# Optimization experiments

Hardware: AMD Instinct MI355X
Metric: run time of the kernel (lower is better)

## Reference

```python
import jax, jax.numpy as jnp
import numpy as np

P_ITER = 30   # Krylov iterations (p_iter=30 in source)
N_PROBE = 100 # stochastic probe vectors (t=100 in source)


def setup_inputs() -> dict:
    N, t, r = 8192, N_PROBE, 256
    key = jax.random.key(0)
    kA, ky, kz = jax.random.split(key, 3)
    # Well-conditioned SPD kernel + noise matrix: K = A A^T / r + I
    A = jax.random.normal(kA, (N, r), dtype=jnp.float32)
    Knn_noise = (A @ A.T) / r + jnp.eye(N, dtype=jnp.float32)
    y = jax.random.normal(ky, (N, 1), dtype=jnp.float32)
    # Rademacher probes (||z||^2 = N exactly)
    Z = jnp.where(jax.random.normal(kz, (N, t)) >= 0, 1.0, -1.0).astype(jnp.float32)
    return {"Knn_noise": Knn_noise, "y": y, "Z": Z}


def _batched_cg(K, B, p_iter):
    """Batched conjugate gradients on K X = B, tracking Lanczos coefficients.
    B: [N, M]. Returns X [N, M], alphas [p, M], betas [p, M]."""
    X = jnp.zeros_like(B)
    R = B
    P = B
    rs = jnp.sum(R * R, axis=0)  # [M]

    def step(carry, _):
        X, R, P, rs = carry
        V = K @ P                               # [N, M] dense matvec (GEMM)
        pv = jnp.sum(P * V, axis=0)             # [M]
        alpha = rs / pv
        X = X + alpha * P
        R = R - alpha * V
        rs_new = jnp.sum(R * R, axis=0)
        beta = rs_new / rs
        P = R + beta * P
        return (X, R, P, rs_new), (alpha, beta)

    (X, _, _, _), (alphas, betas) = jax.lax.scan(step, (X, R, P, rs), None, length=p_iter)
    return X, alphas, betas


def _slq_logdet(alphas, betas, N):
    """Stochastic Lanczos quadrature logdet from CG coefficients.
    alphas, betas: [p, t] (one column per probe)."""
    inv_a = 1.0 / alphas                                   # [p, t]
    diag = inv_a.at[1:].add(betas[:-1] / alphas[:-1])      # T diagonal  [p, t]
    off = jnp.sqrt(betas[:-1]) / alphas[:-1]               # T off-diag  [p-1, t]

    def make_T(d, o):
        return jnp.diag(d) + jnp.diag(o, 1) + jnp.diag(o, -1)

    Ts = jax.vmap(make_T, in_axes=(1, 1))(diag, off)       # [t, p, p]
    lam, V = jnp.linalg.eigh(Ts)                           # small p x p eig per probe
    lam = jnp.maximum(lam, 1e-12)
    # z^T log(K) z ~= ||z||^2 * e1^T Vexp log(Lam) V^T e1 ; ||z||^2 = N (Rademacher)
    quad = jnp.sum(V[:, 0, :] ** 2 * jnp.log(lam), axis=1)  # [t]
    return N * jnp.mean(quad)


def reference(Knn_noise, y, Z):
    N = y.shape[0]
    B = jnp.concatenate([y, Z], axis=1)                    # solve + probes together
    X, alphas, betas = _batched_cg(Knn_noise, B, P_ITER)
    Knn_i_y = X[:, :1]                                     # K^{-1} y
    log_det = _slq_logdet(alphas[:, 1:], betas[:, 1:], N)  # SLQ logdet from probes
    two_pi = jnp.asarray(2.0 * np.pi, dtype=y.dtype)
    return -0.5 * (y.T @ Knn_i_y) - 0.5 * log_det - N * 0.5 * jnp.log(two_pi)
```

## Files before the change

### kernel.cpp

```cpp
#include <hip/hip_runtime.h>
#include <hip/hip_fp16.h>

#define NN 8192
#define NCOLS 101
#define CPW 112
#define BN 128
#define BM 128
#define KSPL 8
#define KCH (NN / KSPL)
#define NSTEP (KCH / 128)
#define PITER 30
#define PVLD 104
#define NSMALL 23424

typedef __attribute__((ext_vector_type(4))) float f32x4;

__device__ __forceinline__ void async_copy16(const void* g, void* l) {
  __builtin_amdgcn_global_load_lds(
      (const __attribute__((address_space(1))) unsigned int*)g,
      (__attribute__((address_space(3))) unsigned int*)l, 16, 0, 0);
}

__device__ __forceinline__ unsigned int pack_fp8x4(float x, float y, float z, float w) {
  unsigned int v = __builtin_amdgcn_cvt_pk_fp8_f32(x, y, 0, false);
  v = __builtin_amdgcn_cvt_pk_fp8_f32(z, w, v, true);
  return v;
}

__device__ __forceinline__ float block_sum(float v) {
  __shared__ float sw[4];
  __syncthreads();
  #pragma unroll
  for (int o = 32; o > 0; o >>= 1) v += __shfl_down(v, o);
  int w = threadIdx.x >> 6;
  if ((threadIdx.x & 63) == 0) sw[w] = v;
  __syncthreads();
  float r = 0.f;
  if (threadIdx.x < 4) r = sw[threadIdx.x];
  r += __shfl_down(r, 2);
  r += __shfl_down(r, 1);
  return r;
}

__global__ __launch_bounds__(256, 2) void gemm_kernel(
    const unsigned char* __restrict__ Kbt,
    const unsigned char* __restrict__ Pb,
    const float* __restrict__ Pf,
    const float* __restrict__ SCit,
    __half* __restrict__ Vp,
    float* __restrict__ pvp) {
  __shared__ __align__(16) unsigned char smem[65536];
  unsigned char* sA = smem;
  unsigned char* sB = smem + 32768;
  float* sC = (float*)smem;

  int bx = blockIdx.x;
  int kz = bx & 7;
  int rb = bx >> 3;
  int tid = threadIdx.x;
  int lane = tid & 63;
  int w = tid >> 6;
  int r0 = rb * BM;
  int k0 = kz * KCH;
  int lrow = lane >> 3;
  int gseg = (lane & 7) ^ lrow;
  int asrc = lrow * 128 + gseg * 16;
  int mm = lane & 15;
  int quad = lane >> 4;
  int q1 = quad >> 1, q0 = quad & 1;
  int wm = w >> 1, wn = w & 1;

  const unsigned char* Apanel = Kbt + ((size_t)bx << 17);

  int aBase[4], aXor[4], bBase[4], bXor[4];
  #pragma unroll
  for (int i = 0; i < 4; ++i) {
    int arow = wm * 64 + i * 16 + mm;
    aBase[i] = arow * 128 + (q0 << 3);
    aXor[i] = (arow & 7) << 4;
    int bcol = wn * 64 + i * 16 + mm;
    bBase[i] = bcol * 128 + (q0 << 3);
    bXor[i] = (bcol & 7) << 4;
  }

  f32x4 acc[4][4];
  #pragma unroll
  for (int i = 0; i < 4; ++i)
    #pragma unroll
    for (int j = 0; j < 4; ++j) acc[i][j] = (f32x4){0.f, 0.f, 0.f, 0.f};

  auto stage = [&](int s, int buf) {
    int kk = k0 + s * 128;
    #pragma unroll
    for (int q = 0; q < 4; ++q) {
      async_copy16(Apanel + (s << 14) + (w * 32 + q * 8) * 128 + asrc,
                   sA + buf * 16384 + (w * 32 + q * 8) * 128);
      async_copy16(Pb + (size_t)(w * 32 + q * 8 + lrow) * NN + kk + gseg * 16,
                   sB + buf * 16384 + (w * 32 + q * 8) * 128);
    }
  };

  stage(0, 0);
  __syncthreads();

  #pragma unroll 2
  for (int s = 0; s < NSTEP; ++s) {
    int cur = s & 1;
    if (s + 1 < NSTEP) stage(s + 1, cur ^ 1);
    const unsigned char* A = sA + cur * 16384;
    const unsigned char* B = sB + cur * 16384;
    #pragma unroll
    for (int kh = 0; kh < 4; ++kh) {
      int s16 = (kh * 2 + q1) << 4;
      long long aF[4], bF[4];
      #pragma unroll
      for (int i = 0; i < 4; ++i) {
        aF[i] = *(const long long*)(A + aBase[i] + (s16 ^ aXor[i]));
        bF[i] = *(const long long*)(B + bBase[i] + (s16 ^ bXor[i]));
      }
      #pragma unroll
      for (int i = 0; i < 4; ++i)
        #pragma unroll
        for (int j = 0; j < 4; ++j)
          acc[i][j] = __builtin_amdgcn_mfma_f32_16x16x32_fp8_fp8(aF[i], bF[j], acc[i][j], 0, 0, 0);
    }
    __syncthreads();
  }
  #pragma unroll
  for (int i = 0; i < 4; ++i)
    #pragma unroll
    for (int j = 0; j < 4; ++j) {
      int ctile = wn * 64 + j * 16;
      if (ctile >= CPW) continue;
      #pragma unroll
      for (int r = 0; r < 4; ++r)
        sC[(wm * 64 + i * 16 + quad * 4 + r) * 113 + ctile + mm] = acc[i][j][r];
    }
  __syncthreads();
  const size_t SPL = (size_t)CPW * NN;
  __half* Vout = Vp + (size_t)kz * SPL;
  for (int idx = tid; idx < BM * CPW; idx += 256) {
    int col = idx >> 7;
    int row = idx & 127;
    if (col < NCOLS)
      Vout[(size_t)col * NN + r0 + row] = __float2half(sC[row * 113 + col] * SCit[col]);
  }
  int rr = tid & 63;
  int g = tid >> 6;
  for (int j = 0; j < 26; ++j) {
    int c = g + j * 4;
    float prod = 0.f;
    if (c < NCOLS)
      prod = (sC[rr * 113 + c] * Pf[(size_t)c * NN + r0 + rr] +
              sC[(rr + 64) * 113 + c] * Pf[(size_t)c * NN + r0 + 64 + rr]) * SCit[c];
    #pragma unroll
    for (int o = 32; o > 0; o >>= 1) prod += __shfl_down(prod, o);
    if (rr == 0 && c < NCOLS) pvp[(size_t)bx * PVLD + c] = prod;
  }
}

__global__ void update1_kernel(const __half* __restrict__ Vp,
                               const float* __restrict__ Pf,
                               float* __restrict__ R,
                               float* __restrict__ X0,
                               const float* __restrict__ pvp,
                               const float* __restrict__ rs,
                               float* __restrict__ rs_new,
                               float* __restrict__ alphas) {
  const size_t SPL = (size_t)CPW * NN;
  __shared__ float s_alpha;
  int c = blockIdx.y;
  int t = threadIdx.x;
  float pvv = pvp[(size_t)t * PVLD + c] + pvp[(size_t)(t + 256) * PVLD + c];
  float pvtot = block_sum(pvv);
  if (t == 0) s_alpha = rs[c] / pvtot;
  __syncthreads();
  float alpha = s_alpha;

  size_t off = (size_t)c * NN + blockIdx.x * 1024 + t * 4;
  float4 v = {0.f, 0.f, 0.f, 0.f};
  #pragma unroll
  for (int sp = 0; sp < KSPL; ++sp) {
    const __half2* p = (const __half2*)(Vp + sp * SPL + off);
    float2 f01 = __half22float2(p[0]);
    float2 f23 = __half22float2(p[1]);
    v.x += f01.x; v.y += f01.y; v.z += f23.x; v.w += f23.y;
  }
  float4 r = *(float4*)(R + off);
  r.x -= alpha * v.x; r.y -= alpha * v.y; r.z -= alpha * v.z; r.w -= alpha * v.w;
  *(float4*)(R + off) = r;
  if (c == 0) {
    size_t xo = blockIdx.x * 1024 + t * 4;
    float4 x = *(float4*)(X0 + xo);
    float4 p = *(const float4*)(Pf + off);
    x.x += alpha * p.x; x.y += alpha * p.y; x.z += alpha * p.z; x.w += alpha * p.w;
    *(float4*)(X0 + xo) = x;
  }
  float rn = r.x * r.x + r.y * r.y + r.z * r.z + r.w * r.w;
  float tot = block_sum(rn);
  if (t == 0) {
    atomicAdd(rs_new + c, tot);
    if (blockIdx.x == 0) alphas[c] = alpha;
  }
}

__global__ void update2_kernel(const float* __restrict__ R,
                               float* __restrict__ P,
                               unsigned char* __restrict__ Pb,
                               const float* __restrict__ rs,
                               const float* __restrict__ rs_new,
                               const float* __restrict__ PNold,
                               float* __restrict__ PNnew,
                               float* __restrict__ SCnew,
                               float* __restrict__ betas) {
  int c = blockIdx.y;
  float rsn = rs_new[c];
  float beta = rsn / rs[c];
  float pnn = rsn + beta * beta * PNold[c];
  float sc = exp2f(roundf(0.5f * log2f(pnn * (1.f / 8192.f))));
  float inv = 1.f / sc;
  size_t off = (size_t)c * NN + blockIdx.x * 1024 + threadIdx.x * 4;
  float4 r = *(const float4*)(R + off);
  float4 p = *(float4*)(P + off);
  p.x = r.x + beta * p.x; p.y = r.y + beta * p.y;
  p.z = r.z + beta * p.z; p.w = r.w + beta * p.w;
  *(float4*)(P + off) = p;
  *(unsigned int*)(Pb + off) = pack_fp8x4(p.x * inv, p.y * inv, p.z * inv, p.w * inv);
  if (threadIdx.x == 0 && blockIdx.x == 0) {
    betas[c] = beta;
    PNnew[c] = pnn;
    SCnew[c] = sc;
  }
}

__global__ void cast_k_kernel(const float* __restrict__ K, unsigned char* __restrict__ Kbt) {
  for (size_t u = (size_t)blockIdx.x * 256 + threadIdx.x; u < (size_t)NN * NN / 16;
       u += (size_t)gridDim.x * 256) {
    size_t d = u * 16;
    int p = (int)(d >> 17);
    int rem = (int)(d & 131071);
    int s = rem >> 14;
    int row = (rem >> 7) & 127;
    int cb = rem & 127;
    int r = (p >> 3) * 128 + row;
    int c = (p & 7) * KCH + s * 128 + cb;
    const float* src = K + (size_t)r * NN + c;
    float4 f0 = *(const float4*)(src);
    float4 f1 = *(const float4*)(src + 4);
    float4 f2 = *(const float4*)(src + 8);
    float4 f3 = *(const float4*)(src + 12);
    uint4 o;
    o.x = pack_fp8x4(f0.x, f0.y, f0.z, f0.w);
    o.y = pack_fp8x4(f1.x, f1.y, f1.z, f1.w);
    o.z = pack_fp8x4(f2.x, f2.y, f2.z, f2.w);
    o.w = pack_fp8x4(f3.x, f3.y, f3.z, f3.w);
    *(uint4*)(Kbt + d) = o;
  }
}

__global__ void init_vec_kernel(const float* __restrict__ y, const float* __restrict__ Z,
                                float* __restrict__ P, float* __restrict__ R,
                                unsigned char* __restrict__ Pb) {
  int c = blockIdx.y;
  int i = blockIdx.x * 256 + threadIdx.x;
  float val = (c == 0) ? y[i] : Z[(size_t)i * 100 + (c - 1)];
  size_t off = (size_t)c * NN + i;
  P[off] = val;
  R[off] = val;
  Pb[off] = (unsigned char)(__builtin_amdgcn_cvt_pk_fp8_f32(val, 0.f, 0, false) & 0xFF);
}

__global__ void init_misc_kernel(float* __restrict__ X0, float* __restrict__ smalls,
                                 unsigned char* __restrict__ Pbpad) {
  const int total = 8192 + NSMALL + 27 * NN;
  for (int t = blockIdx.x * 256 + threadIdx.x; t < total; t += gridDim.x * 256) {
    if (t < 8192) X0[t] = 0.f;
    else if (t < 8192 + NSMALL) smalls[t - 8192] = 0.f;
    else Pbpad[t - (8192 + NSMALL)] = 0;
  }
}

__global__ void init_rs_kernel(const float* __restrict__ y, float* __restrict__ rs0,
                               float* __restrict__ pn0, float* __restrict__ sc0) {
  int t = threadIdx.x;
  float s = 0.f;
  for (int i = t; i < NN; i += 256) { float v = y[i]; s += v * v; }
  float tot = block_sum(s);
  if (t == 0) { rs0[0] = tot; pn0[0] = tot; }
  if (t >= 1 && t <= 100) { rs0[t] = (float)NN; pn0[t] = (float)NN; }
  if (t < 128) sc0[t] = 1.f;
}

__global__ __launch_bounds__(64, 1) void slq_kernel(
    const float* __restrict__ AL, const float* __restrict__ BE,
    float* __restrict__ QP) {
  __shared__ double sd[PITER], se[PITER];
  int lane = threadIdx.x;
  int c = blockIdx.x + 1;
  if (lane < PITER) {
    double a = (double)AL[lane * 128 + c];
    double dd = 1.0 / a;
    if (lane > 0) {
      double ap = (double)AL[(lane - 1) * 128 + c];
      double bp = (double)BE[(lane - 1) * 128 + c];
      dd += bp / ap;
    }
    sd[lane] = dd;
    double ee = 0.0;
    if (lane < PITER - 1) {
      double b = (double)BE[lane * 128 + c];
      ee = sqrt(b) / a;
    }
    se[lane] = ee;
  }
  __syncthreads();
  double d[PITER], e[PITER];
  #pragma unroll
  for (int i = 0; i < PITER; ++i) { d[i] = sd[i]; e[i] = se[i]; }

  float quadk = 0.f;
  if (lane < PITER) {
    double lo = 1e300, hi = -1e300;
    #pragma unroll
    for (int i = 0; i < PITER; ++i) {
      double r = e[i] + (i > 0 ? e[i - 1] : 0.0);
      lo = fmin(lo, d[i] - r);
      hi = fmax(hi, d[i] + r);
    }
    int k = lane;
    for (int it = 0; it < 48; ++it) {
      double mid = 0.5 * (lo + hi);
      int cnt = 0;
      double q = d[0] - mid;
      cnt += (q < 0.0);
      #pragma unroll
      for (int i = 1; i < PITER; ++i) {
        double aq = fabs(q);
        if (aq < 1e-30) q = (q < 0.0) ? -1e-30 : 1e-30;
        q = d[i] - mid - (e[i - 1] * e[i - 1]) / q;
        cnt += (q < 0.0);
      }
      if (cnt > k) hi = mid; else lo = mid;
    }
    double lam = 0.5 * (lo + hi);
    double e0 = fmax(e[0], 1e-150);
    double vprev = 1.0;
    double vcur = (lam - d[0]) / e0;
    double s = 1.0 + vcur * vcur;
    double scale2 = 1.0;
    #pragma unroll
    for (int i = 1; i < PITER - 1; ++i) {
      double ei = fmax(e[i], 1e-150);
      double vnext = ((lam - d[i]) * vcur - e[i - 1] * vprev) / ei;
      if (fabs(vnext) > 1e150) {
        vnext *= 1e-150; vcur *= 1e-150; s *= 1e-300; scale2 *= 1e-300;
      }
      vprev = vcur; vcur = vnext;
      s += vcur * vcur;
    }
    double w = scale2 / s;
    double lc = lam > 1e-12 ? lam : 1e-12;
    quadk = (float)(w * log(lc));
  }
  #pragma unroll
  for (int o = 32; o > 0; o >>= 1) quadk += __shfl_down(quadk, o);
  if (lane == 0) QP[blockIdx.x] = quadk;
}

__global__ void final2_kernel(const float* __restrict__ y, const float* __restrict__ X0,
                              const float* __restrict__ QP, float* __restrict__ out) {
  int t = threadIdx.x;
  float s = 0.f;
  for (int i = t; i < NN; i += 256) s += y[i] * X0[i];
  float ydot = block_sum(s);
  __syncthreads();
  float q = (t < 100) ? QP[t] : 0.f;
  float qsum = block_sum(q);
  if (t == 0) {
    float logdet = (float)NN * (qsum * 0.01f);
    out[0] = -0.5f * ydot - 0.5f * logdet - (float)NN * 0.5f * 1.8378770664093454f;
  }
}

extern "C" void kernel_launch(void* const* d_in, const int* in_sizes, int n_in,
                              void* d_out, int out_size, void* d_ws, size_t ws_size,
                              hipStream_t stream) {
  const float* K = (const float*)d_in[0];
  const float* y = (const float*)d_in[1];
  const float* Z = (const float*)d_in[2];
  float* out = (float*)d_out;
  char* ws = (char*)d_ws;
  if (ws_size < 89796096ull) return;

  unsigned char* Kbt = (unsigned char*)(ws + 0ull);
  unsigned char* Pb = (unsigned char*)(ws + 67108864ull);
  float* P   = (float*)(ws + 68157440ull);
  float* R   = (float*)(ws + 71467008ull);
  __half* Vp = (__half*)(ws + 74776576ull);
  float* X0  = (float*)(ws + 89456640ull);
  float* PVP = (float*)(ws + 89489408ull);
  float* SM  = (float*)(ws + 89702400ull);
  float* RS = SM;
  float* AL = SM + 7808;
  float* BE = SM + 11648;
  float* PN = SM + 15488;
  float* SC = SM + 19456;
  float* QP = (float*)(ws + 74776576ull);

  cast_k_kernel<<<8192, 256, 0, stream>>>(K, Kbt);
  init_vec_kernel<<<dim3(32, 101), 256, 0, stream>>>(y, Z, P, R, Pb);
  init_misc_kernel<<<240, 256, 0, stream>>>(X0, SM, Pb + (size_t)NCOLS * NN);
  init_rs_kernel<<<1, 256, 0, stream>>>(y, RS, PN, SC);

  for (int it = 0; it < PITER; ++it) {
    gemm_kernel<<<512, 256, 0, stream>>>(Kbt, Pb, P, SC + it * 128, Vp, PVP);
    update1_kernel<<<dim3(8, 101), 256, 0, stream>>>(Vp, P, R, X0, PVP,
        RS + it * 128, RS + (it + 1) * 128, AL + it * 128);
    update2_kernel<<<dim3(8, 101), 256, 0, stream>>>(R, P, Pb, RS + it * 128,
        RS + (it + 1) * 128, PN + it * 128, PN + (it + 1) * 128,
        SC + (it + 1) * 128, BE + it * 128);
  }
  slq_kernel<<<100, 64, 0, stream>>>(AL, BE, QP);
  final2_kernel<<<1, 256, 0, stream>>>(y, X0, QP, out);
}
```

Before: 2.032 ms.

## Fuse CG update kernels into one per-column block and merge init kernels

Replaces the two per-iteration update kernels with a single kernel using one 1024-thread block per column. That block reduces the full residual norm itself, so there is no atomicAdd and no second pass that rereads R. It also skips the P update on the last iteration. The four init kernels are merged into one launch. This removes a kernel launch per iteration and an R round-trip through memory, at the cost of only 101 blocks, which may leave many CUs idle for the bandwidth-bound update.

Result: faster. 1.916 ms (-5.7%).

```diff
diff --git a/kernel.cpp b/kernel.cpp
--- a/kernel.cpp
+++ b/kernel.cpp
@@ -11,7 +11,6 @@
 #define NSTEP (KCH / 128)
 #define PITER 30
 #define PVLD 104
-#define NSMALL 23424
 
 typedef __attribute__((ext_vector_type(4))) float f32x4;
 
@@ -37,6 +36,23 @@
   __syncthreads();
   float r = 0.f;
   if (threadIdx.x < 4) r = sw[threadIdx.x];
+  r += __shfl_down(r, 2);
+  r += __shfl_down(r, 1);
+  return r;
+}
+
+__device__ __forceinline__ float block_sum1024(float v) {
+  __shared__ float sw[16];
+  __syncthreads();
+  #pragma unroll
+  for (int o = 32; o > 0; o >>= 1) v += __shfl_down(v, o);
+  int w = threadIdx.x >> 6;
+  if ((threadIdx.x & 63) == 0) sw[w] = v;
+  __syncthreads();
+  float r = 0.f;
+  if (threadIdx.x < 16) r = sw[threadIdx.x];
+  r += __shfl_down(r, 8);
+  r += __shfl_down(r, 4);
   r += __shfl_down(r, 2);
   r += __shfl_down(r, 1);
   return r;
@@ -159,83 +175,96 @@
   }
 }
 
-__global__ void update1_kernel(const __half* __restrict__ Vp,
-                               const float* __restrict__ Pf,
-                               float* __restrict__ R,
-                               float* __restrict__ X0,
-                               const float* __restrict__ pvp,
-                               const float* __restrict__ rs,
-                               float* __restrict__ rs_new,
-                               float* __restrict__ alphas) {
+__global__ __launch_bounds__(1024, 1) void update_kernel(
+    const __half* __restrict__ Vp, float* __restrict__ P,
+    float* __restrict__ R, float* __restrict__ X0,
+    unsigned char* __restrict__ Pb, const float* __restrict__ pvp,
+    float* __restrict__ SM, int it) {
+  float* RS = SM;
+  float* AL = SM + 7808;
+  float* BE = SM + 11648;
+  float* PN = SM + 15488;
+  float* SC = SM + 19456;
+  __shared__ float sbc[2];
+
+  int c = blockIdx.x;
+  int t = threadIdx.x;
   const size_t SPL = (size_t)CPW * NN;
-  __shared__ float s_alpha;
-  int c = blockIdx.y;
+  size_t base = (size_t)c * NN;
+
+  float pvv = (t < 512) ? pvp[(size_t)t * PVLD + c] : 0.f;
+  float pvtot = block_sum1024(pvv);
+  float rs_old = RS[it * 128 + c];
+  if (t == 0) sbc[0] = rs_old / pvtot;
+  __syncthreads();
+  float alpha = sbc[0];
+
+  float4 rv[2];
+  float rn = 0.f;
+  #pragma unroll
+  for (int j = 0; j < 2; ++j) {
+    size_t off = base + j * 4096 + t * 4;
+    float4 v = {0.f, 0.f, 0.f, 0.f};
+    #pragma unroll
+    for (int sp = 0; sp < KSPL; ++sp) {
+      const __half2* ph = (const __half2*)(Vp + sp * SPL + off);
+      float2 f01 = __half22float2(ph[0]);
+      float2 f23 = __half22float2(ph[1]);
+      v.x += f01.x; v.y += f01.y; v.z += f23.x; v.w += f23.y;
+    }
+    float4 r = *(float4*)(R + off);
+    r.x -= alpha * v.x; r.y -= alpha * v.y;
+    r.z -= alpha * v.z; r.w -= alpha * v.w;
+    *(float4*)(R + off) = r;
+    rv[j] = r;
+    rn += r.x * r.x + r.y * r.y + r.z * r.z + r.w * r.w;
+    if (c == 0) {
+      size_t xo = j * 4096 + t * 4;
+      float4 x = *(float4*)(X0 + xo);
+      float4 p = *(const float4*)(P + off);
+      x.x += alpha * p.x; x.y += alpha * p.y;
+      x.z += alpha * p.z; x.w += alpha * p.w;
+      *(float4*)(X0 + xo) = x;
+    }
+  }
+  float rsn = block_sum1024(rn);
+  if (t == 0) {
+    float beta = rsn / rs_old;
+    float pnn = rsn + beta * beta * PN[it * 128 + c];
+    float sc = exp2f(roundf(0.5f * log2f(pnn * (1.f / 8192.f))));
+    AL[it * 128 + c] = alpha;
+    BE[it * 128 + c] = beta;
+    PN[(it + 1) * 128 + c] = pnn;
+    SC[(it + 1) * 128 + c] = sc;
+    RS[(it + 1) * 128 + c] = rsn;
+    sbc[0] = beta;
+    sbc[1] = 1.f / sc;
+  }
+  __syncthreads();
+  if (it < PITER - 1) {
+    float beta = sbc[0], inv = sbc[1];
+    #pragma unroll
+    for (int j = 0; j < 2; ++j) {
+      size_t off = base + j * 4096 + t * 4;
+      float4 p = *(float4*)(P + off);
+      p.x = rv[j].x + beta * p.x; p.y = rv[j].y + beta * p.y;
+      p.z = rv[j].z + beta * p.z; p.w = rv[j].w + beta * p.w;
+      *(float4*)(P + off) = p;
+      *(unsigned int*)(Pb + off) = pack_fp8x4(p.x * inv, p.y * inv, p.z * inv, p.w * inv);
+    }
+  }
+}
+
+__global__ void init_all(const float* __restrict__ K, const float* __restrict__ y,
+                         const float* __restrict__ Z, unsigned char* __restrict__ Kbt,
+                         unsigned char* __restrict__ Pb, float* __restrict__ P,
+                         float* __restrict__ R, float* __restrict__ X0,
+                         float* __restrict__ SM) {
+  int b = blockIdx.x;
   int t = threadIdx.x;
-  float pvv = pvp[(size_t)t * PVLD + c] + pvp[(size_t)(t + 256) * PVLD + c];
-  float pvtot = block_sum(pvv);
-  if (t == 0) s_alpha = rs[c] / pvtot;
-  __syncthreads();
-  float alpha = s_alpha;
-
-  size_t off = (size_t)c * NN + blockIdx.x * 1024 + t * 4;
-  float4 v = {0.f, 0.f, 0.f, 0.f};
-  #pragma unroll
-  for (int sp = 0; sp < KSPL; ++sp) {
-    const __half2* p = (const __half2*)(Vp + sp * SPL + off);
-    float2 f01 = __half22float2(p[0]);
-    float2 f23 = __half22float2(p[1]);
-    v.x += f01.x; v.y += f01.y; v.z += f23.x; v.w += f23.y;
-  }
-  float4 r = *(float4*)(R + off);
-  r.x -= alpha * v.x; r.y -= alpha * v.y; r.z -= alpha * v.z; r.w -= alpha * v.w;
-  *(float4*)(R + off) = r;
-  if (c == 0) {
-    size_t xo = blockIdx.x * 1024 + t * 4;
-    float4 x = *(float4*)(X0 + xo);
-    float4 p = *(const float4*)(Pf + off);
-    x.x += alpha * p.x; x.y += alpha * p.y; x.z += alpha * p.z; x.w += alpha * p.w;
-    *(float4*)(X0 + xo) = x;
-  }
-  float rn = r.x * r.x + r.y * r.y + r.z * r.z + r.w * r.w;
-  float tot = block_sum(rn);
-  if (t == 0) {
-    atomicAdd(rs_new + c, tot);
-    if (blockIdx.x == 0) alphas[c] = alpha;
-  }
-}
-
-__global__ void update2_kernel(const float* __restrict__ R,
-                               float* __restrict__ P,
-                               unsigned char* __restrict__ Pb,
-                               const float* __restrict__ rs,
-                               const float* __restrict__ rs_new,
-                               const float* __restrict__ PNold,
-                               float* __restrict__ PNnew,
-                               float* __restrict__ SCnew,
-                               float* __restrict__ betas) {
-  int c = blockIdx.y;
-  float rsn = rs_new[c];
-  float beta = rsn / rs[c];
-  float pnn = rsn + beta * beta * PNold[c];
-  float sc = exp2f(roundf(0.5f * log2f(pnn * (1.f / 8192.f))));
-  float inv = 1.f / sc;
-  size_t off = (size_t)c * NN + blockIdx.x * 1024 + threadIdx.x * 4;
-  float4 r = *(const float4*)(R + off);
-  float4 p = *(float4*)(P + off);
-  p.x = r.x + beta * p.x; p.y = r.y + beta * p.y;
-  p.z = r.z + beta * p.z; p.w = r.w + beta * p.w;
-  *(float4*)(P + off) = p;
-  *(unsigned int*)(Pb + off) = pack_fp8x4(p.x * inv, p.y * inv, p.z * inv, p.w * inv);
-  if (threadIdx.x == 0 && blockIdx.x == 0) {
-    betas[c] = beta;
-    PNnew[c] = pnn;
-    SCnew[c] = sc;
-  }
-}
-
-__global__ void cast_k_kernel(const float* __restrict__ K, unsigned char* __restrict__ Kbt) {
-  for (size_t u = (size_t)blockIdx.x * 256 + threadIdx.x; u < (size_t)NN * NN / 16;
-       u += (size_t)gridDim.x * 256) {
+  int gid = b * 256 + t;
+  const int gsz = 512 * 256;
+  for (size_t u = gid; u < (size_t)NN * NN / 16; u += gsz) {
     size_t d = u * 16;
     int p = (int)(d >> 17);
     int rem = (int)(d & 131071);
@@ -256,39 +285,30 @@
     o.w = pack_fp8x4(f3.x, f3.y, f3.z, f3.w);
     *(uint4*)(Kbt + d) = o;
   }
-}
-
-__global__ void init_vec_kernel(const float* __restrict__ y, const float* __restrict__ Z,
-                                float* __restrict__ P, float* __restrict__ R,
-                                unsigned char* __restrict__ Pb) {
-  int c = blockIdx.y;
-  int i = blockIdx.x * 256 + threadIdx.x;
-  float val = (c == 0) ? y[i] : Z[(size_t)i * 100 + (c - 1)];
-  size_t off = (size_t)c * NN + i;
-  P[off] = val;
-  R[off] = val;
-  Pb[off] = (unsigned char)(__builtin_amdgcn_cvt_pk_fp8_f32(val, 0.f, 0, false) & 0xFF);
-}
-
-__global__ void init_misc_kernel(float* __restrict__ X0, float* __restrict__ smalls,
-                                 unsigned char* __restrict__ Pbpad) {
-  const int total = 8192 + NSMALL + 27 * NN;
-  for (int t = blockIdx.x * 256 + threadIdx.x; t < total; t += gridDim.x * 256) {
-    if (t < 8192) X0[t] = 0.f;
-    else if (t < 8192 + NSMALL) smalls[t - 8192] = 0.f;
-    else Pbpad[t - (8192 + NSMALL)] = 0;
-  }
-}
-
-__global__ void init_rs_kernel(const float* __restrict__ y, float* __restrict__ rs0,
-                               float* __restrict__ pn0, float* __restrict__ sc0) {
-  int t = threadIdx.x;
-  float s = 0.f;
-  for (int i = t; i < NN; i += 256) { float v = y[i]; s += v * v; }
-  float tot = block_sum(s);
-  if (t == 0) { rs0[0] = tot; pn0[0] = tot; }
-  if (t >= 1 && t <= 100) { rs0[t] = (float)NN; pn0[t] = (float)NN; }
-  if (t < 128) sc0[t] = 1.f;
+  for (int v = gid; v < NCOLS * NN; v += gsz) {
+    int c = v >> 13;
+    int i = v & 8191;
+    float val = (c == 0) ? y[i] : Z[(size_t)i * 100 + (c - 1)];
+    size_t off = (size_t)c * NN + i;
+    P[off] = val;
+    R[off] = val;
+    Pb[off] = (unsigned char)(__builtin_amdgcn_cvt_pk_fp8_f32(val, 0.f, 0, false) & 0xFF);
+  }
+  for (int i = gid; i < 8192 + 27 * NN; i += gsz) {
+    if (i < 8192) X0[i] = 0.f;
+    else Pb[(size_t)NCOLS * NN + (i - 8192)] = 0;
+  }
+  if (b == 511) {
+    float* RS = SM;
+    float* PN = SM + 15488;
+    float* SC = SM + 19456;
+    float s = 0.f;
+    for (int i = t; i < NN; i += 256) { float v = y[i]; s += v * v; }
+    float tot = block_sum(s);
+    if (t == 0) { RS[0] = tot; PN[0] = tot; }
+    if (t >= 1 && t <= 100) { RS[t] = (float)NN; PN[t] = (float)NN; }
+    if (t < 128) SC[t] = 1.f;
+  }
 }
 
 __global__ __launch_bounds__(64, 1) void slq_kernel(
@@ -400,25 +420,16 @@
   float* X0  = (float*)(ws + 89456640ull);
   float* PVP = (float*)(ws + 89489408ull);
   float* SM  = (float*)(ws + 89702400ull);
-  float* RS = SM;
   float* AL = SM + 7808;
   float* BE = SM + 11648;
-  float* PN = SM + 15488;
   float* SC = SM + 19456;
   float* QP = (float*)(ws + 74776576ull);
 
-  cast_k_kernel<<<8192, 256, 0, stream>>>(K, Kbt);
-  init_vec_kernel<<<dim3(32, 101), 256, 0, stream>>>(y, Z, P, R, Pb);
-  init_misc_kernel<<<240, 256, 0, stream>>>(X0, SM, Pb + (size_t)NCOLS * NN);
-  init_rs_kernel<<<1, 256, 0, stream>>>(y, RS, PN, SC);
+  init_all<<<512, 256, 0, stream>>>(K, y, Z, Kbt, Pb, P, R, X0, SM);
 
   for (int it = 0; it < PITER; ++it) {
     gemm_kernel<<<512, 256, 0, stream>>>(Kbt, Pb, P, SC + it * 128, Vp, PVP);
-    update1_kernel<<<dim3(8, 101), 256, 0, stream>>>(Vp, P, R, X0, PVP,
-        RS + it * 128, RS + (it + 1) * 128, AL + it * 128);
-    update2_kernel<<<dim3(8, 101), 256, 0, stream>>>(R, P, Pb, RS + it * 128,
-        RS + (it + 1) * 128, PN + it * 128, PN + (it + 1) * 128,
-        SC + (it + 1) * 128, BE + it * 128);
+    update_kernel<<<NCOLS, 1024, 0, stream>>>(Vp, P, R, X0, Pb, PVP, SM, it);
   }
   slq_kernel<<<100, 64, 0, stream>>>(AL, BE, QP);
   final2_kernel<<<1, 256, 0, stream>>>(y, X0, QP, out);
```
